# Performance work log

Measured on AMD Instinct MI355X. Metric: run time of the kernel, lower is better.

## Reference

```python
import jax, jax.numpy as jnp
import numpy as np

HIDDEN = 4096
INTER = 11008
B, S = 8, 16
QMAX = 127  # int8 symmetric range for w_bits=8


def setup_inputs() -> dict:
    key = jax.random.key(0)
    ks = jax.random.split(key, 7)
    hidden_state = jax.random.normal(ks[0], (B, S, HIDDEN), dtype=jnp.float32)
    # Quantized weights stored as integer values in float32 (as the dequant source)
    w1_q = jax.random.randint(ks[1], (INTER, HIDDEN), -QMAX - 1, QMAX + 1).astype(jnp.float32)
    w3_q = jax.random.randint(ks[2], (INTER, HIDDEN), -QMAX - 1, QMAX + 1).astype(jnp.float32)
    w2_q = jax.random.randint(ks[3], (HIDDEN, INTER), -QMAX - 1, QMAX + 1).astype(jnp.float32)
    # Per-output-channel dequant scales (has_scale=True)
    w1_s = jax.random.uniform(ks[4], (INTER,), dtype=jnp.float32, minval=0.5, maxval=1.5) * 0.01
    w3_s = jax.random.uniform(ks[5], (INTER,), dtype=jnp.float32, minval=0.5, maxval=1.5) * 0.01
    w2_s = jax.random.uniform(ks[6], (HIDDEN,), dtype=jnp.float32, minval=0.5, maxval=1.5) * 0.01
    return {"hidden_state": hidden_state, "w1_q": w1_q, "w1_s": w1_s,
            "w3_q": w3_q, "w3_s": w3_s, "w2_q": w2_q, "w2_s": w2_s}


def _dequant_linear(x, w_q, w_s):
    # w_q: [out, in] integer-valued weights; w_s: [out] per-channel scale
    # y = x @ (w_q * w_s[:, None]).T == (x @ w_q.T) * w_s
    return jnp.einsum('bsh,oh->bso', x, w_q) * w_s


def reference(hidden_state, w1_q, w1_s, w3_q, w3_s, w2_q, w2_s):
    up = _dequant_linear(hidden_state, w1_q, w1_s)      # [B,S,INTER]
    gate = _dequant_linear(hidden_state, w3_q, w3_s)    # [B,S,INTER]
    h = jax.nn.silu(up) * gate                          # SwiGLU
    return _dequant_linear(h, w2_q, w2_s)               # [B,S,HIDDEN]
```

## Files before the change

kernel.cpp:

```cpp
#include <hip/hip_runtime.h>

#define HIDDEN 4096
#define INTER  11008
#define MTOK   128
#define NMERG  (2*INTER)
#define KS1    1
#define KS2    4
#define SK     256
#define RST    1040
#define TILE   (32*RST)

typedef short          short8  __attribute__((ext_vector_type(8)));
typedef unsigned short ushort8 __attribute__((ext_vector_type(8)));
typedef float          f32x16  __attribute__((ext_vector_type(16)));
#define AS1 __attribute__((address_space(1)))
#define AS3 __attribute__((address_space(3)))

static __device__ __forceinline__ unsigned short f2bf_rne(float f) {
    unsigned u = __builtin_bit_cast(unsigned, f);
    u += 0x7FFFu + ((u >> 16) & 1u);
    return (unsigned short)(u >> 16);
}
static __device__ __forceinline__ float bf2f(unsigned short b) {
    unsigned u = (unsigned)b << 16;
    return __builtin_bit_cast(float, u);
}
static __device__ __forceinline__ int pk2(float lo, float hi) {
    return (int)__builtin_amdgcn_perm(__builtin_bit_cast(unsigned, hi),
                                      __builtin_bit_cast(unsigned, lo),
                                      0x07060302u);
}

__global__ void cvt_x_k(const float* __restrict__ x, unsigned short* __restrict__ A2) {
    int f = blockIdx.x * 256 + threadIdx.x;
    int lane = f & 63, w = f >> 6;
    int kstep = w >> 2, ms = w & 3;
    int m = ms * 32 + (lane & 31);
    int k = kstep * 16 + (lane >> 5) * 8;
    const float* src = x + (size_t)m * HIDDEN + k;
    float4 v0 = *(const float4*)(src);
    float4 v1 = *(const float4*)(src + 4);
    ushort8 o;
    o[0] = f2bf_rne(v0.x); o[1] = f2bf_rne(v0.y); o[2] = f2bf_rne(v0.z); o[3] = f2bf_rne(v0.w);
    o[4] = f2bf_rne(v1.x); o[5] = f2bf_rne(v1.y); o[6] = f2bf_rne(v1.z); o[7] = f2bf_rne(v1.w);
    *(ushort8*)(A2 + (size_t)f * 8) = o;
}

template<bool OBF16>
__global__ __launch_bounds__(256) void gemm_k(
    const unsigned short* __restrict__ A2,
    const float* __restrict__ B0, const float* __restrict__ B1, int nhalf,
    void* __restrict__ part, int K, int N, int totTiles, int ksplit)
{
    __shared__ __align__(16) char lds[2 * TILE];
    const int lane = threadIdx.x & 63;
    const int ws   = threadIdx.x >> 6;
    const int n0   = blockIdx.x * 32;
    const int ks   = blockIdx.y;
    const int tbeg = (ks * totTiles) / ksplit;
    const int tend = ((ks + 1) * totTiles) / ksplit;
    const int nt   = tend - tbeg;

    const char* rowp[8];
#pragma unroll
    for (int r = 0; r < 8; ++r) {
        int n = n0 + ws * 8 + r;
        const float* p = (n < nhalf) ? B0 + (size_t)n * K
                                     : B1 + (size_t)(n - nhalf) * K;
        rowp[r] = (const char*)p + lane * 16;
    }

    f32x16 acc;
#pragma unroll
    for (int r = 0; r < 16; ++r) acc[r] = 0.f;

    auto stage = [&](int t, int buf) {
        const size_t koff = (size_t)t * (SK * 4);
#pragma unroll
        for (int r = 0; r < 8; ++r) {
            __builtin_amdgcn_global_load_lds(
                (const AS1 unsigned*)(rowp[r] + koff),
                (AS3 unsigned*)(lds + buf * TILE + (ws * 8 + r) * RST), 16, 0, 0);
        }
    };
    auto loadA = [&](int t, short8 (&Ar)[16]) {
#pragma unroll
        for (int s = 0; s < 16; ++s) {
            int kg = t * 16 + s;
            Ar[s] = *(const short8*)(A2 + ((size_t)(kg * 4 + ws) * 64 + lane) * 8);
        }
    };

    short8 A0v[16], A1v[16];

    auto iter = [&](int i, short8 (&Ar)[16]) {
        if (i + 1 < nt) { asm volatile("s_waitcnt vmcnt(24)" ::: "memory"); }
        else            { asm volatile("s_waitcnt vmcnt(0)"  ::: "memory"); }
        __builtin_amdgcn_sched_barrier(0);
        __builtin_amdgcn_s_barrier();

        const char* lb = lds + (size_t)(i & 1) * TILE
                       + (lane & 31) * RST + (lane >> 5) * 32;
#pragma unroll
        for (int s = 0; s < 16; ++s) {
            float4 v0 = *(const float4*)(lb + s * 64);
            float4 v1 = *(const float4*)(lb + s * 64 + 16);
            int4 bi;
            bi.x = pk2(v0.x, v0.y); bi.y = pk2(v0.z, v0.w);
            bi.z = pk2(v1.x, v1.y); bi.w = pk2(v1.z, v1.w);
            short8 bf = __builtin_bit_cast(short8, bi);
            acc = __builtin_amdgcn_mfma_f32_32x32x16_bf16(Ar[s], bf, acc, 0, 0, 0);
        }

        asm volatile("s_waitcnt lgkmcnt(0)" ::: "memory");
        __builtin_amdgcn_sched_barrier(0);
        __builtin_amdgcn_s_barrier();
        if (i + 2 < nt) { stage(tbeg + i + 2, i & 1); loadA(tbeg + i + 2, Ar); }
    };

    stage(tbeg, 0); loadA(tbeg, A0v);
    if (nt > 1) { stage(tbeg + 1, 1); loadA(tbeg + 1, A1v); }

    for (int i = 0; i < nt; i += 2) {
        iter(i, A0v);
        if (i + 1 < nt) iter(i + 1, A1v);
    }

    const int n = n0 + (lane & 31);
#pragma unroll
    for (int r = 0; r < 16; ++r) {
        int m = ws * 32 + (r & 3) + 8 * (r >> 2) + 4 * (lane >> 5);
        size_t idx = ((size_t)ks * MTOK + m) * (size_t)N + n;
        if (OBF16) ((unsigned short*)part)[idx] = f2bf_rne(acc[r]);
        else       ((float*)part)[idx] = acc[r];
    }
}

__global__ void swiglu_k(const unsigned short* __restrict__ p1,
                         const float* __restrict__ s1, const float* __restrict__ s3,
                         unsigned short* __restrict__ h2)
{
    int f = blockIdx.x * 256 + threadIdx.x;
    int lane = f & 63, w = f >> 6;
    int kstep = w >> 2, ms = w & 3;
    int m = ms * 32 + (lane & 31);
    int j = kstep * 16 + (lane >> 5) * 8;
    float up[8], gt[8];
#pragma unroll
    for (int e = 0; e < 8; ++e) { up[e] = 0.f; gt[e] = 0.f; }
#pragma unroll
    for (int ks = 0; ks < KS1; ++ks) {
        const unsigned short* pu = p1 + ((size_t)ks * MTOK + m) * NMERG + j;
        ushort8 u = *(const ushort8*)(pu);
        ushort8 g = *(const ushort8*)(pu + INTER);
#pragma unroll
        for (int e = 0; e < 8; ++e) { up[e] += bf2f(u[e]); gt[e] += bf2f(g[e]); }
    }
    float4 c1a = *(const float4*)(s1 + j), c1b = *(const float4*)(s1 + j + 4);
    float4 c3a = *(const float4*)(s3 + j), c3b = *(const float4*)(s3 + j + 4);
    float c1[8] = {c1a.x, c1a.y, c1a.z, c1a.w, c1b.x, c1b.y, c1b.z, c1b.w};
    float c3[8] = {c3a.x, c3a.y, c3a.z, c3a.w, c3b.x, c3b.y, c3b.z, c3b.w};
    ushort8 o;
#pragma unroll
    for (int e = 0; e < 8; ++e) {
        float u = up[e] * c1[e], g = gt[e] * c3[e];
        o[e] = f2bf_rne(g * u / (1.f + __expf(-u)));
    }
    *(ushort8*)(h2 + (size_t)f * 8) = o;
}

__global__ void reduce_k(const float* __restrict__ p, const float* __restrict__ s2,
                         float* __restrict__ out)
{
    int i = (blockIdx.x * 256 + threadIdx.x) * 4;
    float4 acc = *(const float4*)(p + i);
#pragma unroll
    for (int s = 1; s < KS2; ++s) {
        float4 v = *(const float4*)(p + (size_t)s * MTOK * HIDDEN + i);
        acc.x += v.x; acc.y += v.y; acc.z += v.z; acc.w += v.w;
    }
    int ncol = i & (HIDDEN - 1);
    float4 sc = *(const float4*)(s2 + ncol);
    acc.x *= sc.x; acc.y *= sc.y; acc.z *= sc.z; acc.w *= sc.w;
    *(float4*)(out + i) = acc;
}

extern "C" void kernel_launch(void* const* d_in, const int* in_sizes, int n_in,
                              void* d_out, int out_size, void* d_ws, size_t ws_size,
                              hipStream_t stream) {
    const float* x   = (const float*)d_in[0];
    const float* w1q = (const float*)d_in[1];
    const float* w1s = (const float*)d_in[2];
    const float* w3q = (const float*)d_in[3];
    const float* w3s = (const float*)d_in[4];
    const float* w2q = (const float*)d_in[5];
    const float* w2s = (const float*)d_in[6];
    float* out = (float*)d_out;

    char* ws = (char*)d_ws;
    unsigned short* xb2 = (unsigned short*)ws;
    unsigned short* h2  = (unsigned short*)(ws + (1u << 20));
    void* part          = (void*)(ws + (4u << 20));

    cvt_x_k<<<MTOK * HIDDEN / 8 / 256, 256, 0, stream>>>(x, xb2);
    gemm_k<true><<<dim3(NMERG / 32, KS1), 256, 0, stream>>>(
        xb2, w1q, w3q, INTER, part, HIDDEN, NMERG, HIDDEN / SK, KS1);
    swiglu_k<<<MTOK * INTER / 8 / 256, 256, 0, stream>>>(
        (const unsigned short*)part, w1s, w3s, h2);
    gemm_k<false><<<dim3(HIDDEN / 32, KS2), 256, 0, stream>>>(
        h2, w2q, w2q, 1 << 30, part, INTER, HIDDEN, INTER / SK, KS2);
    reduce_k<<<MTOK * HIDDEN / 4 / 256, 256, 0, stream>>>(
        (const float*)part, w2s, out);
}
```

Measured before the change: 513.7 us.

## Convert fp32 integer weights to packed int8 before GEMMs

Adds a kernel that packs the integer-valued fp32 weights into int8 bytes in workspace. Both GEMMs now stream the int8 weights into LDS with 4-byte loads and expand them to bf16 in registers before the MFMA. The intent is to cut the bytes each GEMM reads and the LDS footprint. The conversion runs on every call and must itself read all the fp32 weights, so total memory traffic rises by the extra int8 write and read.

Result: slower. 577.3 us (+12.4%).

```diff
diff --git a/kernel.cpp b/kernel.cpp
--- a/kernel.cpp
+++ b/kernel.cpp
@@ -6,9 +6,9 @@
 #define NMERG  (2*INTER)
 #define KS1    1
 #define KS2    4
-#define SK     256
-#define RST    1040
-#define TILE   (32*RST)
+#define SKB    256
+#define RSTB   272
+#define TILEB  (32*RSTB)
 
 typedef short          short8  __attribute__((ext_vector_type(8)));
 typedef unsigned short ushort8 __attribute__((ext_vector_type(8)));
@@ -29,6 +29,19 @@
     return (int)__builtin_amdgcn_perm(__builtin_bit_cast(unsigned, hi),
                                       __builtin_bit_cast(unsigned, lo),
                                       0x07060302u);
+}
+
+__global__ void wconv_k(const float* __restrict__ src, unsigned* __restrict__ dst) {
+    size_t i = (size_t)blockIdx.x * 256 + threadIdx.x;
+    const float* s = src + i * 8;
+    float4 v0 = *(const float4*)(s);
+    float4 v1 = *(const float4*)(s + 4);
+    unsigned lo = ((unsigned)(int)v0.x & 0xff) | (((unsigned)(int)v0.y & 0xff) << 8) |
+                  (((unsigned)(int)v0.z & 0xff) << 16) | (((unsigned)(int)v0.w) << 24);
+    unsigned hi = ((unsigned)(int)v1.x & 0xff) | (((unsigned)(int)v1.y & 0xff) << 8) |
+                  (((unsigned)(int)v1.z & 0xff) << 16) | (((unsigned)(int)v1.w) << 24);
+    uint2 o; o.x = lo; o.y = hi;
+    *(uint2*)(dst + i * 2) = o;
 }
 
 __global__ void cvt_x_k(const float* __restrict__ x, unsigned short* __restrict__ A2) {
@@ -49,10 +62,11 @@
 template<bool OBF16>
 __global__ __launch_bounds__(256) void gemm_k(
     const unsigned short* __restrict__ A2,
-    const float* __restrict__ B0, const float* __restrict__ B1, int nhalf,
-    void* __restrict__ part, int K, int N, int totTiles, int ksplit)
+    const char* __restrict__ Bq,
+    void* __restrict__ part, int K , int N,
+    int totTiles, int ksplit)
 {
-    __shared__ __align__(16) char lds[2 * TILE];
+    __shared__ __align__(16) char lds[2 * TILEB];
     const int lane = threadIdx.x & 63;
     const int ws   = threadIdx.x >> 6;
     const int n0   = blockIdx.x * 32;
@@ -63,24 +77,20 @@
 
     const char* rowp[8];
 #pragma unroll
-    for (int r = 0; r < 8; ++r) {
-        int n = n0 + ws * 8 + r;
-        const float* p = (n < nhalf) ? B0 + (size_t)n * K
-                                     : B1 + (size_t)(n - nhalf) * K;
-        rowp[r] = (const char*)p + lane * 16;
-    }
+    for (int r = 0; r < 8; ++r)
+        rowp[r] = Bq + (size_t)(n0 + ws * 8 + r) * K + lane * 4;
 
     f32x16 acc;
 #pragma unroll
     for (int r = 0; r < 16; ++r) acc[r] = 0.f;
 
     auto stage = [&](int t, int buf) {
-        const size_t koff = (size_t)t * (SK * 4);
+        const size_t koff = (size_t)t * SKB;
 #pragma unroll
         for (int r = 0; r < 8; ++r) {
             __builtin_amdgcn_global_load_lds(
                 (const AS1 unsigned*)(rowp[r] + koff),
-                (AS3 unsigned*)(lds + buf * TILE + (ws * 8 + r) * RST), 16, 0, 0);
+                (AS3 unsigned*)(lds + buf * TILEB + (ws * 8 + r) * RSTB), 4, 0, 0);
         }
     };
     auto loadA = [&](int t, short8 (&Ar)[16]) {
@@ -99,15 +109,22 @@
         __builtin_amdgcn_sched_barrier(0);
         __builtin_amdgcn_s_barrier();
 
-        const char* lb = lds + (size_t)(i & 1) * TILE
-                       + (lane & 31) * RST + (lane >> 5) * 32;
+        const char* lb = lds + (size_t)(i & 1) * TILEB
+                       + (lane & 31) * RSTB + (lane >> 5) * 8;
 #pragma unroll
         for (int s = 0; s < 16; ++s) {
-            float4 v0 = *(const float4*)(lb + s * 64);
-            float4 v1 = *(const float4*)(lb + s * 64 + 16);
+            uint2 d = *(const uint2*)(lb + s * 16);
+            float f0 = (float)(signed char)(d.x);
+            float f1 = (float)(signed char)(d.x >> 8);
+            float f2 = (float)(signed char)(d.x >> 16);
+            float f3 = (float)(signed char)(d.x >> 24);
+            float f4 = (float)(signed char)(d.y);
+            float f5 = (float)(signed char)(d.y >> 8);
+            float f6 = (float)(signed char)(d.y >> 16);
+            float f7 = (float)(signed char)(d.y >> 24);
             int4 bi;
-            bi.x = pk2(v0.x, v0.y); bi.y = pk2(v0.z, v0.w);
-            bi.z = pk2(v1.x, v1.y); bi.w = pk2(v1.z, v1.w);
+            bi.x = pk2(f0, f1); bi.y = pk2(f2, f3);
+            bi.z = pk2(f4, f5); bi.w = pk2(f6, f7);
             short8 bf = __builtin_bit_cast(short8, bi);
             acc = __builtin_amdgcn_mfma_f32_32x32x16_bf16(Ar[s], bf, acc, 0, 0, 0);
         }
@@ -197,18 +214,26 @@
     const float* w2s = (const float*)d_in[6];
     float* out = (float*)d_out;
 
+    const size_t WB = (size_t)INTER * HIDDEN;
+
     char* ws = (char*)d_ws;
     unsigned short* xb2 = (unsigned short*)ws;
     unsigned short* h2  = (unsigned short*)(ws + (1u << 20));
     void* part          = (void*)(ws + (4u << 20));
-
+    char* wi8           = (char*)(ws + (16u << 20));
+
+    const int NCONV = (int)(WB / 8 / 256);
+
+    wconv_k<<<NCONV, 256, 0, stream>>>(w1q, (unsigned*)wi8);
+    wconv_k<<<NCONV, 256, 0, stream>>>(w3q, (unsigned*)(wi8 + WB));
     cvt_x_k<<<MTOK * HIDDEN / 8 / 256, 256, 0, stream>>>(x, xb2);
     gemm_k<true><<<dim3(NMERG / 32, KS1), 256, 0, stream>>>(
-        xb2, w1q, w3q, INTER, part, HIDDEN, NMERG, HIDDEN / SK, KS1);
+        xb2, wi8, part, HIDDEN, NMERG, HIDDEN / SKB, KS1);
     swiglu_k<<<MTOK * INTER / 8 / 256, 256, 0, stream>>>(
         (const unsigned short*)part, w1s, w3s, h2);
+    wconv_k<<<NCONV, 256, 0, stream>>>(w2q, (unsigned*)wi8);
     gemm_k<false><<<dim3(HIDDEN / 32, KS2), 256, 0, stream>>>(
-        h2, w2q, w2q, 1 << 30, part, INTER, HIDDEN, INTER / SK, KS2);
+        h2, wi8, part, INTER, HIDDEN, INTER / SKB, KS2);
     reduce_k<<<MTOK * HIDDEN / 4 / 256, 256, 0, stream>>>(
         (const float*)part, w2s, out);
 }
```
